# Performance work log

Hardware: AMD Instinct MI355X
Metric: run time of the kernel (lower is better)

Reference implementation:

```python
import jax, jax.numpy as jnp
import numpy as np

N_NODES = 100000
N_EDGES = 1600000
FEAT = 32
HID = 32
N_GRAPHS = 64


def setup_inputs() -> dict:
    key = jax.random.key(0)
    ks = jax.random.split(key, 12)
    x = jax.random.normal(ks[0], (N_NODES, FEAT), dtype=jnp.float32)
    edge_index = jax.random.randint(ks[1], (2, N_EDGES), 0, N_NODES, dtype=jnp.int64)
    batch = jnp.sort(jax.random.randint(ks[2], (N_NODES,), 0, N_GRAPHS, dtype=jnp.int64))
    # ChebConv (K=3) params: one linear per Chebyshev order + shared bias
    W_cheb = jax.random.normal(ks[3], (3, FEAT, HID), dtype=jnp.float32) * 0.1
    b_cheb = jnp.zeros((HID,), dtype=jnp.float32)
    # MLP head 32 -> 1024 -> 512 -> 4
    W1 = jax.random.normal(ks[4], (HID, 1024), dtype=jnp.float32) * 0.05
    b1 = jnp.zeros((1024,), dtype=jnp.float32)
    W2 = jax.random.normal(ks[5], (1024, 512), dtype=jnp.float32) * 0.05
    b2 = jnp.zeros((512,), dtype=jnp.float32)
    W3 = jax.random.normal(ks[6], (512, 4), dtype=jnp.float32) * 0.05
    b3 = jnp.zeros((4,), dtype=jnp.float32)
    return {"x": x, "edge_index": edge_index, "batch": batch,
            "W_cheb": W_cheb, "b_cheb": b_cheb,
            "W1": W1, "b1": b1, "W2": W2, "b2": b2, "W3": W3, "b3": b3}


def reference(x, edge_index, batch, W_cheb, b_cheb, W1, b1, W2, b2, W3, b3):
    row, col = edge_index[0], edge_index[1]  # source, target
    n = x.shape[0]
    # symmetric normalization of scaled Laplacian (lambda_max=2, no self loops):
    # L_hat = -D^{-1/2} A D^{-1/2}
    deg = jax.ops.segment_sum(jnp.ones((row.shape[0],), x.dtype), row, num_segments=n)
    dis = jnp.where(deg > 0, jax.lax.rsqrt(jnp.where(deg > 0, deg, 1.0)), 0.0)
    norm = -(dis[row] * dis[col])  # [E]

    def prop(h):  # L_hat @ h via gather -> scale -> scatter-add
        return jax.ops.segment_sum(norm[:, None] * h[row], col, num_segments=n)

    # Chebyshev recursion: T0=x, T1=L_hat x, T2=2 L_hat T1 - T0
    Tx0 = x
    Tx1 = prop(Tx0)
    Tx2 = 2.0 * prop(Tx1) - Tx0
    h = Tx0 @ W_cheb[0] + Tx1 @ W_cheb[1] + Tx2 @ W_cheb[2] + b_cheb  # [N, HID]
    # global max pool per graph
    g = jax.ops.segment_max(h, batch, num_segments=N_GRAPHS)  # [B, HID]
    # MLP head (dropout/LeakyReLU defined but unused in original forward)
    h1 = jax.nn.relu(g @ W1 + b1)
    h2 = jax.nn.relu(h1 @ W2 + b2)
    return h2 @ W3 + b3  # [B, 4]
```

## Files before the change

kernel.cpp:

```cpp
#include <hip/hip_runtime.h>
#include <hip/hip_fp16.h>


#define NT 256
#define NTS 1024
#define BSHIFT 8
#define BSIZE 256
#define HB 256
#define CAPC 48
#define CAPR 64
#define CAP 5120

typedef _Float16 half8 __attribute__((ext_vector_type(8)));
typedef float f32x4 __attribute__((ext_vector_type(4)));

__device__ __forceinline__ void atomicMaxFloat(float* addr, float val) {
    if (val >= 0.0f) atomicMax((int*)addr, __float_as_int(val));
    else             atomicMin((unsigned int*)addr, __float_as_uint(val));
}

#define ACC8(raw)                                        \
    do {                                                 \
        const __half2* hp_ = (const __half2*)&(raw);     \
        float2 f0_ = __half22float2(hp_[0]);             \
        float2 f1_ = __half22float2(hp_[1]);             \
        float2 f2_ = __half22float2(hp_[2]);             \
        float2 f3_ = __half22float2(hp_[3]);             \
        a0 += f0_.x; a1 += f0_.y; a2 += f1_.x; a3 += f1_.y; \
        a4 += f2_.x; a5 += f2_.y; a6 += f3_.x; a7 += f3_.y; \
    } while (0)

__global__ __launch_bounds__(512) void k_init(float* __restrict__ g,
                                              const float* __restrict__ Wc,
                                              _Float16* __restrict__ wfrag,
                                              int* __restrict__ bcur,
                                              int* __restrict__ rcur, int NBK) {
    int tid = threadIdx.x;
    for (int i = tid; i < 64 * 32; i += 512) g[i] = -__builtin_inff();
    if (tid < 384) {
        int combo = tid >> 6, lane = tid & 63;
        int mat = combo >> 1, n = combo & 1;
        int m = lane & 15, quad = lane >> 4;
        #pragma unroll
        for (int j = 0; j < 8; j++)
            wfrag[(size_t)combo * 512 + lane * 8 + j] =
                (_Float16)Wc[mat * 1024 + (quad * 8 + j) * 32 + n * 16 + m];
    }
    if (tid < NBK) {
        bcur[tid] = tid * CAP;
        rcur[tid] = tid * CAP;
    }
}

__global__ __launch_bounds__(NTS) void k_bscatter(const int* __restrict__ row,
                                                  const int* __restrict__ col,
                                                  int* __restrict__ bcur,
                                                  int* __restrict__ rcur,
                                                  int* __restrict__ ebuck,
                                                  unsigned char* __restrict__ rbuck,
                                                  int E, int NBK, int epb) {
    __shared__ int cntc[512], cntr[512];
    __shared__ int basec[512], baser[512];
    __shared__ int cstage[512 * CAPC];
    __shared__ unsigned char rstage[512 * CAPR];
    int tid = threadIdx.x;
    if (tid < 512) { cntc[tid] = 0; cntr[tid] = 0; }
    __syncthreads();
    int start = blockIdx.x * epb;
    int end = min(start + epb, E);
    for (int e = start + tid; e < end; e += NTS) {
        int r = row[e], c = col[e];
        int bc_ = c >> BSHIFT;
        int li = atomicAdd(&cntc[bc_], 1);
        if (li < CAPC)
            cstage[bc_ * CAPC + li] = (r << BSHIFT) | (c & (BSIZE - 1));
        int br_ = r >> BSHIFT;
        int lj = atomicAdd(&cntr[br_], 1);
        if (lj < CAPR)
            rstage[br_ * CAPR + lj] = (unsigned char)(r & (BSIZE - 1));
    }
    __syncthreads();
    if (tid < 512) {
        int n = min(cntc[tid], CAPC);
        basec[tid] = n ? atomicAdd(&bcur[tid], n) : 0;
    } else {
        int b = tid - 512;
        int n = min(cntr[b], CAPR);
        baser[b] = n ? atomicAdd(&rcur[b], n) : 0;
    }
    __syncthreads();
    int warp = tid >> 6, lane = tid & 63;
    for (int b = warp; b < NBK; b += (NTS >> 6)) {
        int n = min(cntc[b], CAPC);
        int base = basec[b];
        for (int i = lane; i < n; i += 64)
            ebuck[base + i] = cstage[b * CAPC + i];
    }
    for (int b = warp; b < NBK; b += (NTS >> 6)) {
        int n = min(cntr[b], CAPR);
        int base = baser[b];
        for (int i = lane; i < n; i += 64)
            rbuck[base + i] = rstage[b * CAPR + i];
    }
}

__global__ __launch_bounds__(NT) void k_prep(
    const int* __restrict__ rcur, const unsigned char* __restrict__ rbuck,
    const int* __restrict__ bcur, const int* __restrict__ ebuck,
    const float* __restrict__ x,
    float* __restrict__ dis, float* __restrict__ rdis,
    __half* __restrict__ xh, __half* __restrict__ xsh,
    int* __restrict__ offs, int* __restrict__ entries, int N) {
    __shared__ int cnt[1024];
    __shared__ int wsum[4];
    __shared__ float sdis[256];
    int b = blockIdx.x, tid = threadIdx.x;
    int rbase = b * CAP, rend = rcur[b];
    int ebase = b * CAP, eend = bcur[b];
    cnt[tid] = 0; cnt[tid + 256] = 0; cnt[tid + 512] = 0; cnt[tid + 768] = 0;
    __syncthreads();
    for (int e = rbase + tid; e < rend; e += NT)
        atomicAdd(&cnt[rbuck[e]], 1);
    __syncthreads();
    int dcount = cnt[tid];
    int node = (b << BSHIFT) + tid;
    float d = (dcount > 0) ? rsqrtf((float)dcount) : 0.0f;
    if (node < N) {
        dis[node] = d;
        rdis[node] = (dcount > 0) ? sqrtf((float)dcount) : 0.0f;
    }
    sdis[tid] = d;
    __syncthreads();
    cnt[tid] = 0; cnt[tid + 256] = 0; cnt[tid + 512] = 0; cnt[tid + 768] = 0;
    __syncthreads();
    for (int e = ebase + tid; e < eend; e += NT) {
        int pv = ebuck[e];
        atomicAdd(&cnt[((pv & (BSIZE - 1)) << 2) | ((pv >> BSHIFT) >> 15)], 1);
    }
    __syncthreads();
    int s0 = cnt[tid * 4], s1 = cnt[tid * 4 + 1], s2 = cnt[tid * 4 + 2], s3 = cnt[tid * 4 + 3];
    int tot = s0 + s1 + s2 + s3;
    int lane = tid & 63, wv = tid >> 6;
    int v = tot;
    #pragma unroll
    for (int off = 1; off < 64; off <<= 1) {
        int t = __shfl_up(v, off);
        if (lane >= off) v += t;
    }
    if (lane == 63) wsum[wv] = v;
    __syncthreads();
    int wbase = 0;
    #pragma unroll
    for (int i = 0; i < 3; i++) wbase += (i < wv) ? wsum[i] : 0;
    int excl = (v - tot) + wbase;
    if (node < N) offs[node] = ((ebase + excl) << 9) | tot;
    cnt[tid * 4]     = ebase + excl;
    cnt[tid * 4 + 1] = ebase + excl + s0;
    cnt[tid * 4 + 2] = ebase + excl + s0 + s1;
    cnt[tid * 4 + 3] = ebase + excl + s0 + s1 + s2;
    __syncthreads();
    for (int e = ebase + tid; e < eend; e += NT) {
        int pv = ebuck[e];
        int src = pv >> BSHIFT;
        int li = atomicAdd(&cnt[((pv & (BSIZE - 1)) << 2) | (src >> 15)], 1);
        entries[li] = src;
    }
    int nodebase = b << BSHIFT;
    for (int i4 = tid; i4 < 2048; i4 += NT) {
        int gnode = nodebase + (i4 >> 3);
        if (gnode >= N) break;
        float4 v4 = ((const float4*)x)[(size_t)nodebase * 8 + i4];
        float dd = sdis[i4 >> 3];
        float2 o, os;
        ((__half2*)&o)[0] = __floats2half2_rn(v4.x, v4.y);
        ((__half2*)&o)[1] = __floats2half2_rn(v4.z, v4.w);
        ((__half2*)&os)[0] = __floats2half2_rn(dd * v4.x, dd * v4.y);
        ((__half2*)&os)[1] = __floats2half2_rn(dd * v4.z, dd * v4.w);
        ((float2*)xh)[(size_t)nodebase * 8 + i4] = o;
        ((float2*)xsh)[(size_t)nodebase * 8 + i4] = os;
    }
}

__global__ __launch_bounds__(NT) void k_prop1(const int* __restrict__ offs,
                                              const int* __restrict__ entries,
                                              const float* __restrict__ dis,
                                              const __half* __restrict__ xsh,
                                              __half* __restrict__ xs2h, int N) {
    int idx = blockIdx.x * blockDim.x + threadIdx.x;
    int node = idx >> 4, spq = (idx >> 2) & 3, q = idx & 3;
    if (node >= N) return;
    int pv = offs[node];
    int s = pv >> 9, deg = pv & 511;
    int lo = s + ((deg * spq) >> 2);
    int hi = s + ((deg * (spq + 1)) >> 2);
    float a0 = 0, a1 = 0, a2 = 0, a3 = 0, a4 = 0, a5 = 0, a6 = 0, a7 = 0;
    int e = lo;
    for (; e + 4 <= hi; e += 4) {
        int r0 = entries[e], r1 = entries[e + 1], r2 = entries[e + 2], r3 = entries[e + 3];
        float4 w0 = *(const float4*)(xsh + (size_t)r0 * 32 + q * 8);
        float4 w1 = *(const float4*)(xsh + (size_t)r1 * 32 + q * 8);
        float4 w2 = *(const float4*)(xsh + (size_t)r2 * 32 + q * 8);
        float4 w3 = *(const float4*)(xsh + (size_t)r3 * 32 + q * 8);
        ACC8(w0); ACC8(w1); ACC8(w2); ACC8(w3);
    }
    for (; e < hi; e++) {
        int r = entries[e];
        float4 w = *(const float4*)(xsh + (size_t)r * 32 + q * 8);
        ACC8(w);
    }
    a0 += __shfl_xor(a0, 4); a1 += __shfl_xor(a1, 4);
    a2 += __shfl_xor(a2, 4); a3 += __shfl_xor(a3, 4);
    a4 += __shfl_xor(a4, 4); a5 += __shfl_xor(a5, 4);
    a6 += __shfl_xor(a6, 4); a7 += __shfl_xor(a7, 4);
    a0 += __shfl_xor(a0, 8); a1 += __shfl_xor(a1, 8);
    a2 += __shfl_xor(a2, 8); a3 += __shfl_xor(a3, 8);
    a4 += __shfl_xor(a4, 8); a5 += __shfl_xor(a5, 8);
    a6 += __shfl_xor(a6, 8); a7 += __shfl_xor(a7, 8);
    if (spq == 0) {
        float d = dis[node];
        float sd = -d * d;
        float4 ov;
        ((__half2*)&ov)[0] = __floats2half2_rn(sd * a0, sd * a1);
        ((__half2*)&ov)[1] = __floats2half2_rn(sd * a2, sd * a3);
        ((__half2*)&ov)[2] = __floats2half2_rn(sd * a4, sd * a5);
        ((__half2*)&ov)[3] = __floats2half2_rn(sd * a6, sd * a7);
        *(float4*)(xs2h + (size_t)node * 32 + q * 8) = ov;
    }
}

__global__ __launch_bounds__(NT) void k_combine_f(
    const int* __restrict__ offs, const int* __restrict__ entries,
    const float* __restrict__ dis, const float* __restrict__ rdis,
    const __half* __restrict__ xs2h, const _Float16* __restrict__ xh,
    const _Float16* __restrict__ wfrag, const float* __restrict__ bc,
    const int* __restrict__ batch, float* __restrict__ g, int N) {
    __shared__ float sb[32];
    __shared__ float sp2[32][33];
    __shared__ float hs[32][33];
    __shared__ float lmax[64][32];
    __shared__ int sbatch[32];
    __shared__ int s_blo, s_bhi;

    int tid = threadIdx.x;
    if (tid < 32) sb[tid] = bc[tid];
    int rowbase = blockIdx.x * 32;
    if (tid >= 64 && tid < 96) {
        int gr = rowbase + tid - 64;
        sbatch[tid - 64] = (gr < N) ? batch[gr] : -1;
    }

    int node_l = tid >> 3, sp = (tid >> 2) & 1, q = tid & 3;
    int gnode = rowbase + node_l;
    if (gnode < N) {
        int pv = offs[gnode];
        int s = pv >> 9, deg = pv & 511;
        int mid = s + (deg >> 1), t = s + deg;
        int lo = sp ? mid : s;
        int hi = sp ? t : mid;
        float a0 = 0, a1 = 0, a2 = 0, a3 = 0, a4 = 0, a5 = 0, a6 = 0, a7 = 0;
        int e = lo;
        for (; e + 4 <= hi; e += 4) {
            int r0 = entries[e], r1 = entries[e + 1], r2 = entries[e + 2], r3 = entries[e + 3];
            float4 w0 = *(const float4*)(xs2h + (size_t)r0 * 32 + q * 8);
            float4 w1 = *(const float4*)(xs2h + (size_t)r1 * 32 + q * 8);
            float4 w2 = *(const float4*)(xs2h + (size_t)r2 * 32 + q * 8);
            float4 w3 = *(const float4*)(xs2h + (size_t)r3 * 32 + q * 8);
            ACC8(w0); ACC8(w1); ACC8(w2); ACC8(w3);
        }
        for (; e < hi; e++) {
            int r = entries[e];
            float4 w = *(const float4*)(xs2h + (size_t)r * 32 + q * 8);
            ACC8(w);
        }
        a0 += __shfl_xor(a0, 4); a1 += __shfl_xor(a1, 4);
        a2 += __shfl_xor(a2, 4); a3 += __shfl_xor(a3, 4);
        a4 += __shfl_xor(a4, 4); a5 += __shfl_xor(a5, 4);
        a6 += __shfl_xor(a6, 4); a7 += __shfl_xor(a7, 4);
        if (sp == 0) {
            float sc = -dis[gnode];
            float* p = &sp2[node_l][q * 8];
            p[0] = sc * a0; p[1] = sc * a1; p[2] = sc * a2; p[3] = sc * a3;
            p[4] = sc * a4; p[5] = sc * a5; p[6] = sc * a6; p[7] = sc * a7;
        }
    }
    __syncthreads();

    int wave = tid >> 6;
    int lane = tid & 63;
    int m = lane & 15;
    int quad = lane >> 4;
    if (wave < 2) {
        int grow = rowbase + wave * 16 + m;
        half8 a0 = {}, a1 = {}, a2 = {};
        if (grow < N) {
            size_t off = (size_t)grow * 32 + quad * 8;
            a0 = *(const half8*)(xh + off);
            half8 x2 = *(const half8*)((const _Float16*)xs2h + off);
            float rd = rdis[grow];
            const float* p = &sp2[wave * 16 + m][quad * 8];
            #pragma unroll
            for (int j = 0; j < 8; j++) {
                a1[j] = (_Float16)((float)x2[j] * rd);
                a2[j] = (_Float16)(2.0f * p[j] - (float)a0[j]);
            }
        }
        const half8* wf = (const half8*)wfrag;
        f32x4 acc[2];
        #pragma unroll
        for (int n = 0; n < 2; n++) {
            f32x4 c = {0.f, 0.f, 0.f, 0.f};
            c = __builtin_amdgcn_mfma_f32_16x16x32_f16(a0, wf[(0 * 2 + n) * 64 + lane], c, 0, 0, 0);
            c = __builtin_amdgcn_mfma_f32_16x16x32_f16(a1, wf[(1 * 2 + n) * 64 + lane], c, 0, 0, 0);
            c = __builtin_amdgcn_mfma_f32_16x16x32_f16(a2, wf[(2 * 2 + n) * 64 + lane], c, 0, 0, 0);
            acc[n] = c;
        }
        #pragma unroll
        for (int n = 0; n < 2; n++)
            #pragma unroll
            for (int r = 0; r < 4; r++)
                hs[wave * 16 + quad * 4 + r][n * 16 + m] = acc[n][r] + sb[n * 16 + m];
    }
    if (tid == 0) {
        int lo = sbatch[0];
        int hi = lo;
        for (int j = 31; j > 0; j--) {
            if (sbatch[j] >= 0) { hi = sbatch[j]; break; }
        }
        s_blo = lo; s_bhi = hi;
    }
    __syncthreads();

    int bspan = s_bhi - s_blo + 1;
    for (int i = tid; i < bspan * 32; i += NT) lmax[i >> 5][i & 31] = -__builtin_inff();
    __syncthreads();
    int f = tid & 31, sg = tid >> 5;
    int curb = -1;
    float curm = 0.0f;
    for (int j = sg * 4; j < sg * 4 + 4; j++) {
        int b = sbatch[j];
        if (b < 0) continue;
        float v = hs[j][f];
        if (b != curb) {
            if (curb >= 0) atomicMaxFloat(&lmax[curb - s_blo][f], curm);
            curb = b;
            curm = v;
        } else {
            curm = fmaxf(curm, v);
        }
    }
    if (curb >= 0) atomicMaxFloat(&lmax[curb - s_blo][f], curm);
    __syncthreads();
    for (int i = tid; i < bspan * 32; i += NT) {
        float v = lmax[i >> 5][i & 31];
        if (v > -__builtin_inff()) atomicMaxFloat(&g[(s_blo + (i >> 5)) * 32 + (i & 31)], v);
    }
}

__global__ __launch_bounds__(NT) void k_mlp12(const float* __restrict__ g,
                                              const float* __restrict__ W1,
                                              const float* __restrict__ b1,
                                              const float* __restrict__ W2,
                                              float* __restrict__ h2part) {
    __shared__ float sgA[32], sgB[32];
    __shared__ float shA[128], shB[128];
    int gp = blockIdx.x >> 3, ks = blockIdx.x & 7;
    int giA = gp * 2, giB = gp * 2 + 1;
    int tid = threadIdx.x;
    if (tid < 32) sgA[tid] = g[giA * 32 + tid];
    else if (tid < 64) sgB[tid - 32] = g[giB * 32 + tid - 32];
    __syncthreads();
    if (tid < 128) {
        int c = ks * 128 + tid;
        float a = b1[c], bacc = b1[c];
        #pragma unroll
        for (int k = 0; k < 32; k++) {
            float wv = W1[k * 1024 + c];
            a += sgA[k] * wv;
            bacc += sgB[k] * wv;
        }
        shA[tid] = fmaxf(a, 0.0f);
        shB[tid] = fmaxf(bacc, 0.0f);
    }
    __syncthreads();
    const float* w = W2 + (size_t)(ks * 128) * 512;
    float accA0 = 0.0f, accA1 = 0.0f, accB0 = 0.0f, accB1 = 0.0f;
    for (int k = 0; k < 128; k++) {
        float w0 = w[k * 512 + tid];
        float w1 = w[k * 512 + tid + 256];
        float hA = shA[k], hB = shB[k];
        accA0 += hA * w0; accA1 += hA * w1;
        accB0 += hB * w0; accB1 += hB * w1;
    }
    h2part[giA * 4096 + ks * 512 + tid] = accA0;
    h2part[giA * 4096 + ks * 512 + tid + 256] = accA1;
    h2part[giB * 4096 + ks * 512 + tid] = accB0;
    h2part[giB * 4096 + ks * 512 + tid + 256] = accB1;
}

__global__ __launch_bounds__(NT) void k_mlp3p(const float* __restrict__ h2part,
                                              const float* __restrict__ b2,
                                              const float* __restrict__ W3,
                                              const float* __restrict__ b3,
                                              float* __restrict__ out) {
    __shared__ float sh2[512];
    __shared__ float sp[256];
    int gi = blockIdx.x;
    int tid = threadIdx.x;
    for (int k = tid; k < 512; k += NT) {
        float s = 0.0f;
        #pragma unroll
        for (int p = 0; p < 8; p++) s += h2part[gi * 4096 + p * 512 + k];
        sh2[k] = fmaxf(s + b2[k], 0.0f);
    }
    __syncthreads();
    int j = tid & 3, slot = tid >> 2;
    float part = 0.0f;
    #pragma unroll
    for (int kk = 0; kk < 8; kk++) {
        int k = slot * 8 + kk;
        part += sh2[k] * W3[k * 4 + j];
    }
    sp[tid] = part;
    __syncthreads();
    for (int s = 32; s >= 1; s >>= 1) {
        if (slot < s) sp[tid] += sp[(slot + s) * 4 + j];
        __syncthreads();
    }
    if (slot == 0) out[gi * 4 + j] = sp[j] + b3[j];
}

extern "C" void kernel_launch(void* const* d_in, const int* in_sizes, int n_in,
                              void* d_out, int out_size, void* d_ws, size_t ws_size,
                              hipStream_t stream) {
    const float* x   = (const float*)d_in[0];
    const int* ei    = (const int*)d_in[1];
    const int* batch = (const int*)d_in[2];
    const float* Wc  = (const float*)d_in[3];
    const float* bc  = (const float*)d_in[4];
    const float* W1  = (const float*)d_in[5];
    const float* b1  = (const float*)d_in[6];
    const float* W2  = (const float*)d_in[7];
    const float* b2  = (const float*)d_in[8];
    const float* W3  = (const float*)d_in[9];
    const float* b3  = (const float*)d_in[10];
    float* out       = (float*)d_out;

    const int N = in_sizes[2];
    const int E = in_sizes[1] / 2;
    const int* row = ei;
    const int* col = ei + E;
    const int NBK = (N + BSIZE - 1) / BSIZE;
    const int epb = (E + HB - 1) / HB;
    const size_t PADE = (size_t)NBK * CAP;

    float* h2part   = (float*)d_ws;
    int* bcur       = (int*)(h2part + 64 * 4096);
    int* rcur       = bcur + 512;
    float* dis      = (float*)(rcur + 512);
    float* rdis     = dis + N;
    int* offs       = (int*)(rdis + N);
    int* ebuck      = offs + N + 4;
    unsigned char* rbuck = (unsigned char*)(ebuck + PADE);
    int* entries    = (int*)(rbuck + PADE);
    _Float16* xh    = (_Float16*)(entries + PADE);
    _Float16* xsh   = xh + (size_t)N * 32;
    _Float16* xs2h  = xsh + (size_t)N * 32;
    float* g        = (float*)(xs2h + (size_t)N * 32);
    _Float16* wfrag = (_Float16*)(g + 64 * 32);

    k_init<<<1, 512, 0, stream>>>(g, Wc, wfrag, bcur, rcur, NBK);
    k_bscatter<<<HB, NTS, 0, stream>>>(row, col, bcur, rcur, ebuck, rbuck, E, NBK, epb);
    k_prep<<<NBK, NT, 0, stream>>>(rcur, rbuck, bcur, ebuck, x, dis, rdis,
                                   (__half*)xh, (__half*)xsh, offs, entries, N);
    k_prop1<<<((size_t)N * 16 + NT - 1) / NT, NT, 0, stream>>>(offs, entries, dis, (const __half*)xsh, (__half*)xs2h, N);
    k_combine_f<<<(N + 31) / 32, NT, 0, stream>>>(offs, entries, dis, rdis, (const __half*)xs2h, xh, wfrag, bc, batch, g, N);
    k_mlp12<<<256, NT, 0, stream>>>(g, W1, b1, W2, h2part);
    k_mlp3p<<<64, NT, 0, stream>>>(h2part, b2, W3, b3, out);
}
```

Measured before the change: 192.6 us.

## Split half-precision feature tables into two 16-column halves for gather passes

```diff
diff --git a/kernel.cpp b/kernel.cpp
--- a/kernel.cpp
+++ b/kernel.cpp
@@ -19,15 +19,12 @@
     else             atomicMin((unsigned int*)addr, __float_as_uint(val));
 }
 
-#define ACC8(raw)                                        \
+#define ACC4(raw)                                        \
     do {                                                 \
         const __half2* hp_ = (const __half2*)&(raw);     \
         float2 f0_ = __half22float2(hp_[0]);             \
         float2 f1_ = __half22float2(hp_[1]);             \
-        float2 f2_ = __half22float2(hp_[2]);             \
-        float2 f3_ = __half22float2(hp_[3]);             \
         a0 += f0_.x; a1 += f0_.y; a2 += f1_.x; a3 += f1_.y; \
-        a4 += f2_.x; a5 += f2_.y; a6 += f3_.x; a7 += f3_.y; \
     } while (0)
 
 __global__ __launch_bounds__(512) void k_init(float* __restrict__ g,
@@ -109,7 +106,7 @@
     const int* __restrict__ bcur, const int* __restrict__ ebuck,
     const float* __restrict__ x,
     float* __restrict__ dis, float* __restrict__ rdis,
-    __half* __restrict__ xh, __half* __restrict__ xsh,
+    __half* __restrict__ xh, __half* __restrict__ xsh0, __half* __restrict__ xsh1,
     int* __restrict__ offs, int* __restrict__ entries, int N) {
     __shared__ int cnt[1024];
     __shared__ int wsum[4];
@@ -169,6 +166,7 @@
     for (int i4 = tid; i4 < 2048; i4 += NT) {
         int gnode = nodebase + (i4 >> 3);
         if (gnode >= N) break;
+        int c8 = i4 & 7;
         float4 v4 = ((const float4*)x)[(size_t)nodebase * 8 + i4];
         float dd = sdis[i4 >> 3];
         float2 o, os;
@@ -177,110 +175,106 @@
         ((__half2*)&os)[0] = __floats2half2_rn(dd * v4.x, dd * v4.y);
         ((__half2*)&os)[1] = __floats2half2_rn(dd * v4.z, dd * v4.w);
         ((float2*)xh)[(size_t)nodebase * 8 + i4] = o;
-        ((float2*)xsh)[(size_t)nodebase * 8 + i4] = os;
+        __half* xp = (c8 < 4) ? xsh0 : xsh1;
+        ((float2*)xp)[(size_t)gnode * 4 + (c8 & 3)] = os;
     }
 }
 
 __global__ __launch_bounds__(NT) void k_prop1(const int* __restrict__ offs,
                                               const int* __restrict__ entries,
                                               const float* __restrict__ dis,
-                                              const __half* __restrict__ xsh,
-                                              __half* __restrict__ xs2h, int N) {
+                                              const __half* __restrict__ xsh0,
+                                              const __half* __restrict__ xsh1,
+                                              __half* __restrict__ xs2h0,
+                                              __half* __restrict__ xs2h1, int N) {
     int idx = blockIdx.x * blockDim.x + threadIdx.x;
-    int node = idx >> 4, spq = (idx >> 2) & 3, q = idx & 3;
+    int node = idx >> 3, sp = (idx >> 2) & 1, q = idx & 3;
     if (node >= N) return;
     int pv = offs[node];
     int s = pv >> 9, deg = pv & 511;
-    int lo = s + ((deg * spq) >> 2);
-    int hi = s + ((deg * (spq + 1)) >> 2);
-    float a0 = 0, a1 = 0, a2 = 0, a3 = 0, a4 = 0, a5 = 0, a6 = 0, a7 = 0;
-    int e = lo;
-    for (; e + 4 <= hi; e += 4) {
-        int r0 = entries[e], r1 = entries[e + 1], r2 = entries[e + 2], r3 = entries[e + 3];
-        float4 w0 = *(const float4*)(xsh + (size_t)r0 * 32 + q * 8);
-        float4 w1 = *(const float4*)(xsh + (size_t)r1 * 32 + q * 8);
-        float4 w2 = *(const float4*)(xsh + (size_t)r2 * 32 + q * 8);
-        float4 w3 = *(const float4*)(xsh + (size_t)r3 * 32 + q * 8);
-        ACC8(w0); ACC8(w1); ACC8(w2); ACC8(w3);
-    }
-    for (; e < hi; e++) {
-        int r = entries[e];
-        float4 w = *(const float4*)(xsh + (size_t)r * 32 + q * 8);
-        ACC8(w);
-    }
-    a0 += __shfl_xor(a0, 4); a1 += __shfl_xor(a1, 4);
-    a2 += __shfl_xor(a2, 4); a3 += __shfl_xor(a3, 4);
-    a4 += __shfl_xor(a4, 4); a5 += __shfl_xor(a5, 4);
-    a6 += __shfl_xor(a6, 4); a7 += __shfl_xor(a7, 4);
-    a0 += __shfl_xor(a0, 8); a1 += __shfl_xor(a1, 8);
-    a2 += __shfl_xor(a2, 8); a3 += __shfl_xor(a3, 8);
-    a4 += __shfl_xor(a4, 8); a5 += __shfl_xor(a5, 8);
-    a6 += __shfl_xor(a6, 8); a7 += __shfl_xor(a7, 8);
-    if (spq == 0) {
-        float d = dis[node];
-        float sd = -d * d;
-        float4 ov;
-        ((__half2*)&ov)[0] = __floats2half2_rn(sd * a0, sd * a1);
-        ((__half2*)&ov)[1] = __floats2half2_rn(sd * a2, sd * a3);
-        ((__half2*)&ov)[2] = __floats2half2_rn(sd * a4, sd * a5);
-        ((__half2*)&ov)[3] = __floats2half2_rn(sd * a6, sd * a7);
-        *(float4*)(xs2h + (size_t)node * 32 + q * 8) = ov;
+    int mid = s + (deg >> 1), t = s + deg;
+    int lo = sp ? mid : s;
+    int hi = sp ? t : mid;
+    float d = dis[node];
+    float sd = -d * d;
+    #pragma unroll
+    for (int p = 0; p < 2; p++) {
+        const __half* xp = p ? xsh1 : xsh0;
+        __half* op = p ? xs2h1 : xs2h0;
+        float a0 = 0, a1 = 0, a2 = 0, a3 = 0;
+        int e = lo;
+        for (; e + 4 <= hi; e += 4) {
+            int r0 = entries[e], r1 = entries[e + 1], r2 = entries[e + 2], r3 = entries[e + 3];
+            float2 w0 = *(const float2*)(xp + (size_t)r0 * 16 + q * 4);
+            float2 w1 = *(const float2*)(xp + (size_t)r1 * 16 + q * 4);
+            float2 w2 = *(const float2*)(xp + (size_t)r2 * 16 + q * 4);
+            float2 w3 = *(const float2*)(xp + (size_t)r3 * 16 + q * 4);
+            ACC4(w0); ACC4(w1); ACC4(w2); ACC4(w3);
+        }
+        for (; e < hi; e++) {
+            int r = entries[e];
+            float2 w = *(const float2*)(xp + (size_t)r * 16 + q * 4);
+            ACC4(w);
+        }
+        a0 += __shfl_xor(a0, 4); a1 += __shfl_xor(a1, 4);
+        a2 += __shfl_xor(a2, 4); a3 += __shfl_xor(a3, 4);
+        if (sp == 0) {
+            float2 ov;
+            ((__half2*)&ov)[0] = __floats2half2_rn(sd * a0, sd * a1);
+            ((__half2*)&ov)[1] = __floats2half2_rn(sd * a2, sd * a3);
+            *(float2*)(op + (size_t)node * 16 + q * 4) = ov;
+        }
     }
 }
 
 __global__ __launch_bounds__(NT) void k_combine_f(
     const int* __restrict__ offs, const int* __restrict__ entries,
     const float* __restrict__ dis, const float* __restrict__ rdis,
-    const __half* __restrict__ xs2h, const _Float16* __restrict__ xh,
+    const __half* __restrict__ xs2h0, const __half* __restrict__ xs2h1,
+    const _Float16* __restrict__ xh,
     const _Float16* __restrict__ wfrag, const float* __restrict__ bc,
     const int* __restrict__ batch, float* __restrict__ g, int N) {
     __shared__ float sb[32];
-    __shared__ float sp2[32][33];
-    __shared__ float hs[32][33];
+    __shared__ float sp2[64][33];
+    __shared__ float hs[64][33];
     __shared__ float lmax[64][32];
-    __shared__ int sbatch[32];
+    __shared__ int sbatch[64];
     __shared__ int s_blo, s_bhi;
 
     int tid = threadIdx.x;
     if (tid < 32) sb[tid] = bc[tid];
-    int rowbase = blockIdx.x * 32;
-    if (tid >= 64 && tid < 96) {
+    int rowbase = blockIdx.x * 64;
+    if (tid >= 64 && tid < 128) {
         int gr = rowbase + tid - 64;
         sbatch[tid - 64] = (gr < N) ? batch[gr] : -1;
     }
 
-    int node_l = tid >> 3, sp = (tid >> 2) & 1, q = tid & 3;
+    int node_l = tid >> 2, q = tid & 3;
     int gnode = rowbase + node_l;
     if (gnode < N) {
         int pv = offs[gnode];
-        int s = pv >> 9, deg = pv & 511;
-        int mid = s + (deg >> 1), t = s + deg;
-        int lo = sp ? mid : s;
-        int hi = sp ? t : mid;
-        float a0 = 0, a1 = 0, a2 = 0, a3 = 0, a4 = 0, a5 = 0, a6 = 0, a7 = 0;
-        int e = lo;
-        for (; e + 4 <= hi; e += 4) {
-            int r0 = entries[e], r1 = entries[e + 1], r2 = entries[e + 2], r3 = entries[e + 3];
-            float4 w0 = *(const float4*)(xs2h + (size_t)r0 * 32 + q * 8);
-            float4 w1 = *(const float4*)(xs2h + (size_t)r1 * 32 + q * 8);
-            float4 w2 = *(const float4*)(xs2h + (size_t)r2 * 32 + q * 8);
-            float4 w3 = *(const float4*)(xs2h + (size_t)r3 * 32 + q * 8);
-            ACC8(w0); ACC8(w1); ACC8(w2); ACC8(w3);
-        }
-        for (; e < hi; e++) {
-            int r = entries[e];
-            float4 w = *(const float4*)(xs2h + (size_t)r * 32 + q * 8);
-            ACC8(w);
-        }
-        a0 += __shfl_xor(a0, 4); a1 += __shfl_xor(a1, 4);
-        a2 += __shfl_xor(a2, 4); a3 += __shfl_xor(a3, 4);
-        a4 += __shfl_xor(a4, 4); a5 += __shfl_xor(a5, 4);
-        a6 += __shfl_xor(a6, 4); a7 += __shfl_xor(a7, 4);
-        if (sp == 0) {
-            float sc = -dis[gnode];
-            float* p = &sp2[node_l][q * 8];
-            p[0] = sc * a0; p[1] = sc * a1; p[2] = sc * a2; p[3] = sc * a3;
-            p[4] = sc * a4; p[5] = sc * a5; p[6] = sc * a6; p[7] = sc * a7;
+        int s = pv >> 9, t = s + (pv & 511);
+        float sc = -dis[gnode];
+        #pragma unroll
+        for (int p = 0; p < 2; p++) {
+            const __half* xp = p ? xs2h1 : xs2h0;
+            float a0 = 0, a1 = 0, a2 = 0, a3 = 0;
+            int e = s;
+            for (; e + 4 <= t; e += 4) {
+                int r0 = entries[e], r1 = entries[e + 1], r2 = entries[e + 2], r3 = entries[e + 3];
+                float2 w0 = *(const float2*)(xp + (size_t)r0 * 16 + q * 4);
+                float2 w1 = *(const float2*)(xp + (size_t)r1 * 16 + q * 4);
+                float2 w2 = *(const float2*)(xp + (size_t)r2 * 16 + q * 4);
+                float2 w3 = *(const float2*)(xp + (size_t)r3 * 16 + q * 4);
+                ACC4(w0); ACC4(w1); ACC4(w2); ACC4(w3);
+            }
+            for (; e < t; e++) {
+                int r = entries[e];
+                float2 w = *(const float2*)(xp + (size_t)r * 16 + q * 4);
+                ACC4(w);
+            }
+            float* pp = &sp2[node_l][p * 16 + q * 4];
+            pp[0] = sc * a0; pp[1] = sc * a1; pp[2] = sc * a2; pp[3] = sc * a3;
         }
     }
     __syncthreads();
@@ -289,41 +283,44 @@
     int lane = tid & 63;
     int m = lane & 15;
     int quad = lane >> 4;
-    if (wave < 2) {
-        int grow = rowbase + wave * 16 + m;
-        half8 a0 = {}, a1 = {}, a2 = {};
-        if (grow < N) {
-            size_t off = (size_t)grow * 32 + quad * 8;
-            a0 = *(const half8*)(xh + off);
-            half8 x2 = *(const half8*)((const _Float16*)xs2h + off);
-            float rd = rdis[grow];
-            const float* p = &sp2[wave * 16 + m][quad * 8];
-            #pragma unroll
-            for (int j = 0; j < 8; j++) {
-                a1[j] = (_Float16)((float)x2[j] * rd);
-                a2[j] = (_Float16)(2.0f * p[j] - (float)a0[j]);
-            }
-        }
-        const half8* wf = (const half8*)wfrag;
-        f32x4 acc[2];
-        #pragma unroll
-        for (int n = 0; n < 2; n++) {
-            f32x4 c = {0.f, 0.f, 0.f, 0.f};
-            c = __builtin_amdgcn_mfma_f32_16x16x32_f16(a0, wf[(0 * 2 + n) * 64 + lane], c, 0, 0, 0);
-            c = __builtin_amdgcn_mfma_f32_16x16x32_f16(a1, wf[(1 * 2 + n) * 64 + lane], c, 0, 0, 0);
-            c = __builtin_amdgcn_mfma_f32_16x16x32_f16(a2, wf[(2 * 2 + n) * 64 + lane], c, 0, 0, 0);
-            acc[n] = c;
-        }
-        #pragma unroll
-        for (int n = 0; n < 2; n++)
-            #pragma unroll
-            for (int r = 0; r < 4; r++)
-                hs[wave * 16 + quad * 4 + r][n * 16 + m] = acc[n][r] + sb[n * 16 + m];
-    }
+    int grow = rowbase + wave * 16 + m;
+
+    half8 a0 = {}, a1 = {}, a2 = {};
+    if (grow < N) {
+        a0 = *(const half8*)(xh + (size_t)grow * 32 + quad * 8);
+        const _Float16* x2p = (quad < 2)
+            ? ((const _Float16*)xs2h0 + (size_t)grow * 16 + quad * 8)
+            : ((const _Float16*)xs2h1 + (size_t)grow * 16 + (quad - 2) * 8);
+        half8 x2 = *(const half8*)x2p;
+        float rd = rdis[grow];
+        const float* p2 = &sp2[wave * 16 + m][quad * 8];
+        #pragma unroll
+        for (int j = 0; j < 8; j++) {
+            a1[j] = (_Float16)((float)x2[j] * rd);
+            a2[j] = (_Float16)(2.0f * p2[j] - (float)a0[j]);
+        }
+    }
+
+    const half8* wf = (const half8*)wfrag;
+    f32x4 acc[2];
+    #pragma unroll
+    for (int n = 0; n < 2; n++) {
+        f32x4 c = {0.f, 0.f, 0.f, 0.f};
+        c = __builtin_amdgcn_mfma_f32_16x16x32_f16(a0, wf[(0 * 2 + n) * 64 + lane], c, 0, 0, 0);
+        c = __builtin_amdgcn_mfma_f32_16x16x32_f16(a1, wf[(1 * 2 + n) * 64 + lane], c, 0, 0, 0);
+        c = __builtin_amdgcn_mfma_f32_16x16x32_f16(a2, wf[(2 * 2 + n) * 64 + lane], c, 0, 0, 0);
+        acc[n] = c;
+    }
+
+    #pragma unroll
+    for (int n = 0; n < 2; n++)
+        #pragma unroll
+        for (int r = 0; r < 4; r++)
+            hs[wave * 16 + quad * 4 + r][n * 16 + m] = acc[n][r] + sb[n * 16 + m];
     if (tid == 0) {
         int lo = sbatch[0];
         int hi = lo;
-        for (int j = 31; j > 0; j--) {
+        for (int j = 63; j > 0; j--) {
             if (sbatch[j] >= 0) { hi = sbatch[j]; break; }
         }
         s_blo = lo; s_bhi = hi;
@@ -336,7 +333,7 @@
     int f = tid & 31, sg = tid >> 5;
     int curb = -1;
     float curm = 0.0f;
-    for (int j = sg * 4; j < sg * 4 + 4; j++) {
+    for (int j = sg * 8; j < sg * 8 + 8; j++) {
         int b = sbatch[j];
         if (b < 0) continue;
         float v = hs[j][f];
@@ -463,17 +460,24 @@
     unsigned char* rbuck = (unsigned char*)(ebuck + PADE);
     int* entries    = (int*)(rbuck + PADE);
     _Float16* xh    = (_Float16*)(entries + PADE);
-    _Float16* xsh   = xh + (size_t)N * 32;
-    _Float16* xs2h  = xsh + (size_t)N * 32;
-    float* g        = (float*)(xs2h + (size_t)N * 32);
+    _Float16* xsh0  = xh + (size_t)N * 32;
+    _Float16* xsh1  = xsh0 + (size_t)N * 16;
+    _Float16* xs2h0 = xsh1 + (size_t)N * 16;
+    _Float16* xs2h1 = xs2h0 + (size_t)N * 16;
+    float* g        = (float*)(xs2h1 + (size_t)N * 16);
     _Float16* wfrag = (_Float16*)(g + 64 * 32);
 
     k_init<<<1, 512, 0, stream>>>(g, Wc, wfrag, bcur, rcur, NBK);
     k_bscatter<<<HB, NTS, 0, stream>>>(row, col, bcur, rcur, ebuck, rbuck, E, NBK, epb);
     k_prep<<<NBK, NT, 0, stream>>>(rcur, rbuck, bcur, ebuck, x, dis, rdis,
-                                   (__half*)xh, (__half*)xsh, offs, entries, N);
-    k_prop1<<<((size_t)N * 16 + NT - 1) / NT, NT, 0, stream>>>(offs, entries, dis, (const __half*)xsh, (__half*)xs2h, N);
-    k_combine_f<<<(N + 31) / 32, NT, 0, stream>>>(offs, entries, dis, rdis, (const __half*)xs2h, xh, wfrag, bc, batch, g, N);
+                                   (__half*)xh, (__half*)xsh0, (__half*)xsh1,
+                                   offs, entries, N);
+    k_prop1<<<((size_t)N * 8 + NT - 1) / NT, NT, 0, stream>>>(
+        offs, entries, dis, (const __half*)xsh0, (const __half*)xsh1,
+        (__half*)xs2h0, (__half*)xs2h1, N);
+    k_combine_f<<<(N + 63) / 64, NT, 0, stream>>>(
+        offs, entries, dis, rdis, (const __half*)xs2h0, (const __half*)xs2h1,
+        xh, wfrag, bc, batch, g, N);
     k_mlp12<<<256, NT, 0, stream>>>(g, W1, b1, W2, h2part);
     k_mlp3p<<<64, NT, 0, stream>>>(h2part, b2, W3, b3, out);
 }
```

Result: slower. 208.9 us (+8.5%).
